# Optimization experiments

Hardware: AMD Instinct MI355X
Metric: run time of the kernel (lower is better)

The kernel has to match this reference:

```python
import jax, jax.numpy as jnp
import numpy as np

N, FIN, C1, C2 = 4096, 6, 1000, 1000
K1, K2, KR = 3, 6, 3
NR, S, NCLS = 20, 205, 40


def pairwise_adj(x):
    # exp(-squared_euclidean_distance), RGCNN pairwise_distance
    inner = -2.0 * jnp.einsum('bnf,bmf->bnm', x, x)
    sq = jnp.sum(x * x, axis=-1, keepdims=True)
    return jnp.exp(-(sq + inner + jnp.swapaxes(sq, 1, 2)))


def knn_sparsify(adj, k):
    # keep top-k similarities per row, zero the rest (get_one_matrix_knn)
    vals, idx = jax.lax.top_k(adj, k)
    B, n, _ = adj.shape
    b = jnp.arange(B)[:, None, None]
    r = jnp.arange(n)[None, :, None]
    return jnp.zeros_like(adj).at[b, r, idx].set(vals)


def get_laplacian(W):
    # normalized Laplacian L = I - D^-1/2 W D^-1/2
    dinv = 1.0 / jnp.sqrt(jnp.sum(W, axis=-1))
    Lnorm = W * dinv[:, :, None] * dinv[:, None, :]
    return jnp.eye(W.shape[-1], dtype=W.dtype)[None] - Lnorm


def cheb_conv(x, L, W, b, K):
    # Chebyshev recursion: Tx0=x, Tx1=Lx, Txk=2L Tx_{k-1} - Tx_{k-2}
    Tx = [x]
    if K > 1:
        Tx.append(jnp.einsum('bnm,bmf->bnf', L, x))
    for _ in range(2, K):
        Tx.append(2.0 * jnp.einsum('bnm,bmf->bnf', L, Tx[-1]) - Tx[-2])
    xhat = jnp.concatenate(Tx, axis=-1)  # [B, N, K*Fin]
    return jnp.einsum('bnf,fo->bno', xhat, W) + b


def setup_inputs() -> dict:
    key = jax.random.key(0)
    ks = jax.random.split(key, 16)
    sc = 0.02
    return {
        'x': jax.random.normal(ks[0], (1, N, FIN), jnp.float32),
        'k': 40,
        'batch_size': 1,
        'num_points': N,
        'vertices_Reeb': jax.random.normal(ks[1], (NR, 3), jnp.float32),
        'laplacian_Reeb': jax.random.normal(ks[2], (NR, NR), jnp.float32),
        'sccs': jax.random.randint(ks[3], (NR, S), 0, N),
        'W1': jax.random.normal(ks[4], (K1 * FIN, C1), jnp.float32) * sc,
        'b1': jnp.zeros((C1,), jnp.float32),
        'W2': jax.random.normal(ks[5], (K2 * C1, C2), jnp.float32) * sc,
        'b2': jnp.zeros((C2,), jnp.float32),
        'Wr': jax.random.normal(ks[6], (KR * C1, C2), jnp.float32) * sc,
        'br': jnp.zeros((C2,), jnp.float32),
        'fc1_w': jax.random.normal(ks[7], (2 * C2, 512), jnp.float32) * sc,
        'fc1_b': jnp.zeros((512,), jnp.float32),
        'fc2_w': jax.random.normal(ks[8], (512, 128), jnp.float32) * sc,
        'fc2_b': jnp.zeros((128,), jnp.float32),
        'fc3_w': jax.random.normal(ks[9], (128, NCLS), jnp.float32) * sc,
        'fc3_b': jnp.zeros((NCLS,), jnp.float32),
    }


def reference(x, k, batch_size, num_points, vertices_Reeb, laplacian_Reeb, sccs,
              W1, b1, W2, b2, Wr, br, fc1_w, fc1_b, fc2_w, fc2_b, fc3_w, fc3_b):
    fro = lambda a: jnp.linalg.norm(a.reshape(-1))
    regs = []
    # dynamic KNN graph + Laplacian (no_grad in original -> stop_gradient)
    L = jax.lax.stop_gradient(get_laplacian(knn_sparsify(pairwise_adj(x), k)))
    out = jax.nn.relu(cheb_conv(x, L, W1, b1, K1))  # [1, N, 1000]
    regs.append(fro(jnp.einsum('bnc,bnm,bmf->bcf', out, L, x)))
    # Reeb pooling: max over each scc's node features (sample 0)
    vfr = jnp.max(out[0][sccs], axis=1)[None]  # [1, 20, 1000]
    L_reeb = laplacian_Reeb[None]
    # second dynamic graph on features
    L2 = jax.lax.stop_gradient(get_laplacian(knn_sparsify(pairwise_adj(out), k)))
    out2 = jax.nn.relu(cheb_conv(out, L2, W2, b2, K2))
    regs.append(fro(jnp.einsum('bnc,bnm,bmf->bcf', out2, L2, x)))
    out_reeb = jax.nn.relu(cheb_conv(vfr, L_reeb, Wr, br, KR))
    out_m = jnp.max(out2, axis=1)       # [1, 1000]
    reeb_m = jnp.max(out_reeb, axis=1)  # [1, 1000]
    of = jnp.concatenate([reeb_m, out_m], axis=1)  # [1, 2000]
    of = jax.nn.relu(of @ fc1_w + fc1_b)
    regs += [jnp.linalg.norm(fc1_w.T[0]) ** 2, fc1_b[0] ** 2]
    of = jax.nn.relu(of @ fc2_w + fc2_b)
    regs += [jnp.linalg.norm(fc2_w.T[0]) ** 2, fc2_b[0] ** 2]
    of = of @ fc3_w + fc3_b  # [1, 40]
    regs += [jnp.linalg.norm(fc3_w.T[0]) ** 2, fc3_b[0] ** 2]
    return of, jnp.stack(regs)
```

## Files before the change

### kernel.cpp

```cpp
#include <hip/hip_runtime.h>
#include <math.h>

#define N4    4096
#define FDIM  6
#define CC    1000
#define KP    1024
#define KP6   (6 * KP)
#define KNN   40
#define NRB   20
#define SSC   205

typedef __attribute__((ext_vector_type(8))) short bf16x8;
typedef __attribute__((ext_vector_type(4))) float f32x4;

__device__ __forceinline__ unsigned short f2bf(float f) {
    unsigned u = __float_as_uint(f);
    u = (u + 0x7fffu + ((u >> 16) & 1u)) >> 16;
    return (unsigned short)u;
}
__device__ __forceinline__ float bf2f(short s) {
    return __uint_as_float(((unsigned)(unsigned short)s) << 16);
}

__device__ __forceinline__ unsigned d2key(float d) {
    unsigned u = __float_as_uint(d);
    return ((int)u < 0) ? u : (~u) ^ 0x80000000u;
}
__device__ __forceinline__ float key2d(unsigned k) {
    unsigned u = (k >> 31) ? k : (~k) ^ 0x80000000u;
    return __uint_as_float(u);
}

__device__ __forceinline__ void gload16(const unsigned short* g, short* l) {
    __builtin_amdgcn_global_load_lds(
        (const __attribute__((address_space(1))) unsigned int*)g,
        (__attribute__((address_space(3))) unsigned int*)l, 16, 0, 0);
}


__global__ __launch_bounds__(256) void sqx_kernel(const float* __restrict__ x,
                                                  float* __restrict__ sq1,
                                                  float* __restrict__ xhat) {
    int n = blockIdx.x * blockDim.x + threadIdx.x;
    if (n >= N4) return;
    float s = 0.f;
#pragma unroll
    for (int f = 0; f < FDIM; ++f) {
        float v = x[n * FDIM + f];
        s += v * v;
        xhat[n * 18 + f] = v;
    }
    sq1[n] = s;
}


#define NHC 8
#define HSTRIDE 257

struct TopkSh {
    unsigned sv[N4];
    int hist[NHC * HSTRIDE];
    int sc[256];
    float red[8];
    unsigned short cidx[N4];
    unsigned s_pfx;
    int s_need, s_cnt, s_m;
};

__device__ __forceinline__ void topk_prep(TopkSh& sh, int t) {
    if (t == 0) { sh.s_pfx = 0u; sh.s_need = KNN; sh.s_cnt = 0; sh.s_m = 0; }
    for (int q = t; q < NHC * HSTRIDE; q += 512) sh.hist[q] = 0;
}

__device__ __forceinline__ void hist_pick(TopkSh& sh, int level, int t, int lane, int w, int nc) {
    if (t < 256) {
        int cnt = 0;
        for (int c = 0; c < nc; ++c) cnt += sh.hist[c * HSTRIDE + t];
        sh.sc[t] = cnt;
    }
    __syncthreads();
    if (w == 0) {
        int need = sh.s_need;
        unsigned pfx = sh.s_pfx;
        int c0 = sh.sc[4 * lane + 0], c1 = sh.sc[4 * lane + 1];
        int c2 = sh.sc[4 * lane + 2], c3 = sh.sc[4 * lane + 3];
        int s = c0 + c1 + c2 + c3;
        int suf = s;
#pragma unroll
        for (int off = 1; off < 64; off <<= 1) {
            int ov = __shfl_down(suf, off, 64);
            if (lane + off < 64) suf += ov;
        }
        int above = suf - s;
        int i3 = above + c3, i2 = i3 + c2, i1 = i2 + c1, i0 = i1 + c0;
        if (i3 >= need && i3 - c3 < need) { sh.s_need = need - (i3 - c3); sh.s_pfx = pfx | ((unsigned)(4 * lane + 3) << level); }
        if (i2 >= need && i2 - c2 < need) { sh.s_need = need - (i2 - c2); sh.s_pfx = pfx | ((unsigned)(4 * lane + 2) << level); }
        if (i1 >= need && i1 - c1 < need) { sh.s_need = need - (i1 - c1); sh.s_pfx = pfx | ((unsigned)(4 * lane + 1) << level); }
        if (i0 >= need && i0 - c0 < need) { sh.s_need = need - (i0 - c0); sh.s_pfx = pfx | ((unsigned)(4 * lane + 0) << level); }
    }
    __syncthreads();
}

template<int LASTLEVEL>
__device__ void topk_core(TopkSh& sh, int n, int* __restrict__ idx,
                          float* __restrict__ val, float* __restrict__ rowsum) {
    int t = threadIdx.x, lane = t & 63, w = t >> 6;
    __syncthreads();
    hist_pick(sh, 24, t, lane, w, NHC);
    unsigned b1 = sh.s_pfx >> 24;

    for (int i = t; i < N4; i += 512) {
        unsigned u = sh.sv[i];
        bool isc = ((u >> 24) >= b1);
        unsigned long long mm = __ballot(isc);
        int cw = __popcll(mm);
        int base = 0;
        if (lane == 0 && cw) base = atomicAdd(&sh.s_m, cw);
        base = __shfl(base, 0);
        if (isc) sh.cidx[base + __popcll(mm & ((1ull << lane) - 1ull))] = (unsigned short)i;
    }
    __syncthreads();
    int mcnt = sh.s_m;

    for (int level = 16; level >= LASTLEVEL; level -= 8) {
        for (int q = t; q < HSTRIDE; q += 512) sh.hist[q] = 0;
        __syncthreads();
        unsigned pfx = sh.s_pfx;
        for (int j = t; j < mcnt; j += 512) {
            unsigned u = sh.sv[sh.cidx[j]];
            if ((u >> (level + 8)) == (pfx >> (level + 8)))
                atomicAdd(&sh.hist[(u >> level) & 255], 1);
        }
        __syncthreads();
        hist_pick(sh, level, t, lane, w, 1);
    }
    unsigned Tbits = sh.s_pfx;
    if (LASTLEVEL == 16) Tbits |= (Tbits & 0x80000000u) ? 0u : 0xFFFFu;
    float Tf = __expf(-key2d(Tbits));
    int needEq = sh.s_need;

    float psum = 0.f;
    for (int j = t; j < mcnt; j += 512) {
        unsigned u = sh.sv[sh.cidx[j]];
        if (u > Tbits) {
            int p = atomicAdd(&sh.s_cnt, 1);
            float v = __expf(-key2d(u));
            idx[(size_t)n * KNN + p] = (int)sh.cidx[j];
            val[(size_t)n * KNN + p] = v;
            psum += v;
        }
    }
#pragma unroll
    for (int o = 32; o; o >>= 1) psum += __shfl_down(psum, o);
    if (lane == 0) sh.red[w] = psum;
    __syncthreads();
    if (t == 0) {
        float s = 0.f;
#pragma unroll
        for (int q = 0; q < 8; ++q) s += sh.red[q];
        rowsum[n] = s + (float)needEq * Tf;
    }

    if (t < 64) {
        int filled = KNN - needEq;
        for (int ib = 0; ib < N4 && filled < KNN; ib += 64) {
            bool eq = (sh.sv[ib + t] == Tbits);
            unsigned long long m = __ballot(eq);
            int pre = __popcll(m & ((1ull << t) - 1ull));
            if (eq && (filled + pre) < KNN) {
                idx[(size_t)n * KNN + filled + pre] = ib + t;
                val[(size_t)n * KNN + filled + pre] = Tf;
            }
            filled += __popcll(m);
        }
    }
}

__global__ __launch_bounds__(512) void topk_fused1(const float* __restrict__ x,
                                                   const float* __restrict__ sq1,
                                                   int* __restrict__ idx, float* __restrict__ val,
                                                   float* __restrict__ rowsum) {
    __shared__ TopkSh sh;
    __shared__ float xn[FDIM];
    __shared__ float sns;
    int n = blockIdx.x;
    int t = threadIdx.x;
    if (t < FDIM) xn[t] = x[n * FDIM + t];
    if (t == FDIM) sns = sq1[n];
    topk_prep(sh, t);
    __syncthreads();
    float x0 = xn[0], x1 = xn[1], x2 = xn[2], x3 = xn[3], x4 = xn[4], x5 = xn[5];
    float sn = sns;
    int* hw = &sh.hist[(t & 7) * HSTRIDE];
    for (int i = t; i < N4; i += 512) {
        const float2* xi = (const float2*)(x + i * FDIM);
        float2 p0 = xi[0], p1 = xi[1], p2 = xi[2];
        float d = x0 * p0.x + x1 * p0.y + x2 * p1.x + x3 * p1.y + x4 * p2.x + x5 * p2.y;
        float e = sn + sq1[i] - 2.f * d;
        unsigned k = d2key(e);
        sh.sv[i] = k;
        atomicAdd(&hw[k >> 24], 1);
    }
    topk_core<0>(sh, n, idx, val, rowsum);
}

__global__ __launch_bounds__(512) void topk_radix(const unsigned short* __restrict__ S,
                                                  int* __restrict__ idx, float* __restrict__ val,
                                                  float* __restrict__ rowsum) {
    __shared__ TopkSh sh;
    int n = blockIdx.x;
    int t = threadIdx.x;
    topk_prep(sh, t);
    const unsigned short* row = S + (size_t)n * N4;
    bf16x8 a = *(const bf16x8*)(row + 8 * t);
    __syncthreads();
    int* hw = &sh.hist[(t & 7) * HSTRIDE];
#pragma unroll
    for (int q = 0; q < 8; ++q) {
        unsigned k = d2key(bf2f(a[q]));
        sh.sv[8 * t + q] = k;
        atomicAdd(&hw[k >> 24], 1);
    }
    topk_core<16>(sh, n, idx, val, rowsum);
}

__global__ __launch_bounds__(256) void wnorm_kernel(float* __restrict__ wv,
                                                    const int* __restrict__ idx,
                                                    const float* __restrict__ rs) {
    int i = blockIdx.x * 256 + threadIdx.x;
    if (i >= N4 * KNN) return;
    int n = i / KNN;
    wv[i] = wv[i] * rsqrtf(rs[n]) * rsqrtf(rs[idx[i]]);
}

__global__ __launch_bounds__(64) void spmv_cheb(const float* __restrict__ Tc,
                                                const float* __restrict__ Tp,
                                                float* __restrict__ Tn,
                                                const int* __restrict__ idx,
                                                const float* __restrict__ wv,
                                                int F, int sC, int sP, int sN,
                                                float a, float b) {
    __shared__ int   si[KNN];
    __shared__ float sw[KNN];
    int n = blockIdx.x;
    if (threadIdx.x < KNN) {
        si[threadIdx.x] = idx[(size_t)n * KNN + threadIdx.x];
        sw[threadIdx.x] = wv[(size_t)n * KNN + threadIdx.x];
    }
    __syncthreads();
    for (int c = threadIdx.x; c < F; c += blockDim.x) {
        float s = 0.f;
#pragma unroll 8
        for (int j = 0; j < KNN; ++j) s += sw[j] * Tc[(size_t)si[j] * sC + c];
        float v = a * (Tc[(size_t)n * sC + c] - s);
        if (b != 0.f) v -= b * Tp[(size_t)n * sP + c];
        Tn[(size_t)n * sN + c] = v;
    }
}

__global__ __launch_bounds__(256) void spmv_cheb_bf(const unsigned short* __restrict__ Tcbf,
                                                    const unsigned short* __restrict__ Tpbf,
                                                    unsigned short* __restrict__ Tnbf,
                                                    const int* __restrict__ idx,
                                                    const float* __restrict__ wv,
                                                    float a, float b) {
    __shared__ int   si[KNN];
    __shared__ float sw[KNN];
    __shared__ float part[3][64][9];
    int n = blockIdx.x;
    int t = threadIdx.x;
    int tt = t & 63, g = t >> 6;
    if (t < KNN) {
        si[t] = idx[(size_t)n * KNN + t];
        sw[t] = wv[(size_t)n * KNN + t];
    }
    __syncthreads();
    int c = blockIdx.y * 512 + tt * 8;
    float acc0 = 0, acc1 = 0, acc2 = 0, acc3 = 0, acc4 = 0, acc5 = 0, acc6 = 0, acc7 = 0;
    int j0 = g * 10;
#pragma unroll
    for (int j = j0; j < j0 + 10; ++j) {
        bf16x8 v = *(const bf16x8*)(Tcbf + (size_t)si[j] * KP6 + c);
        float wj = sw[j];
        acc0 += wj * bf2f(v[0]); acc1 += wj * bf2f(v[1]);
        acc2 += wj * bf2f(v[2]); acc3 += wj * bf2f(v[3]);
        acc4 += wj * bf2f(v[4]); acc5 += wj * bf2f(v[5]);
        acc6 += wj * bf2f(v[6]); acc7 += wj * bf2f(v[7]);
    }
    if (g) {
        float* p = part[g - 1][tt];
        p[0] = acc0; p[1] = acc1; p[2] = acc2; p[3] = acc3;
        p[4] = acc4; p[5] = acc5; p[6] = acc6; p[7] = acc7;
    }
    __syncthreads();
    if (g == 0) {
#pragma unroll
        for (int pg = 0; pg < 3; ++pg) {
            const float* p = part[pg][tt];
            acc0 += p[0]; acc1 += p[1]; acc2 += p[2]; acc3 += p[3];
            acc4 += p[4]; acc5 += p[5]; acc6 += p[6]; acc7 += p[7];
        }
        bf16x8 tc = *(const bf16x8*)(Tcbf + (size_t)n * KP6 + c);
        float o0 = a * (bf2f(tc[0]) - acc0), o1 = a * (bf2f(tc[1]) - acc1);
        float o2 = a * (bf2f(tc[2]) - acc2), o3 = a * (bf2f(tc[3]) - acc3);
        float o4 = a * (bf2f(tc[4]) - acc4), o5 = a * (bf2f(tc[5]) - acc5);
        float o6 = a * (bf2f(tc[6]) - acc6), o7 = a * (bf2f(tc[7]) - acc7);
        if (b != 0.f) {
            bf16x8 tp = *(const bf16x8*)(Tpbf + (size_t)n * KP6 + c);
            o0 -= b * bf2f(tp[0]); o1 -= b * bf2f(tp[1]);
            o2 -= b * bf2f(tp[2]); o3 -= b * bf2f(tp[3]);
            o4 -= b * bf2f(tp[4]); o5 -= b * bf2f(tp[5]);
            o6 -= b * bf2f(tp[6]); o7 -= b * bf2f(tp[7]);
        }
        bf16x8 ob;
        ob[0] = (short)f2bf(o0); ob[1] = (short)f2bf(o1);
        ob[2] = (short)f2bf(o2); ob[3] = (short)f2bf(o3);
        ob[4] = (short)f2bf(o4); ob[5] = (short)f2bf(o5);
        ob[6] = (short)f2bf(o6); ob[7] = (short)f2bf(o7);
        *(bf16x8*)(Tnbf + (size_t)n * KP6 + c) = ob;
    }
}


__global__ __launch_bounds__(256) void cvt_bf16_kernel(const float* __restrict__ in,
                                                       unsigned short* __restrict__ out) {
    int i = blockIdx.x * 256 + threadIdx.x;
    int r = i >> 7, g = i & 127;
    bf16x8 v;
    if (g < 125) {
        float4 a = *(const float4*)(in + (size_t)r * CC + g * 8);
        float4 b = *(const float4*)(in + (size_t)r * CC + g * 8 + 4);
        v[0] = (short)f2bf(a.x); v[1] = (short)f2bf(a.y);
        v[2] = (short)f2bf(a.z); v[3] = (short)f2bf(a.w);
        v[4] = (short)f2bf(b.x); v[5] = (short)f2bf(b.y);
        v[6] = (short)f2bf(b.z); v[7] = (short)f2bf(b.w);
    } else {
#pragma unroll
        for (int q = 0; q < 8; ++q) v[q] = 0;
    }
    *(bf16x8*)(out + (size_t)r * KP6 + g * 8) = v;
}

__global__ __launch_bounds__(256) void w2t_kernel(const float* __restrict__ W2,
                                                  unsigned short* __restrict__ out) {
    __shared__ unsigned short tile[64][65];
    int t = threadIdx.x;
    int k0 = blockIdx.x * 64, n0 = blockIdx.y * 64, s = blockIdx.z;
#pragma unroll
    for (int p = 0; p < 16; ++p) {
        int i = p * 256 + t;
        int kk = i >> 6, nn = i & 63;
        int k = k0 + kk, n = n0 + nn;
        float v = (k < CC && n < CC) ? W2[((size_t)s * CC + k) * CC + n] : 0.f;
        tile[kk][nn] = f2bf(v);
    }
    __syncthreads();
#pragma unroll
    for (int p = 0; p < 16; ++p) {
        int i = p * 256 + t;
        int nn = i >> 6, kk = i & 63;
        out[(size_t)(n0 + nn) * KP6 + (size_t)s * KP + k0 + kk] = tile[kk][nn];
    }
}


#define LDT 32
#define SP2 136
#define SP 264
#define ABUF (128 * LDT)
#define BBUF (256 * LDT)

template<int STR>
__device__ __forceinline__ void gemm_core128_bk64(const unsigned short* __restrict__ Ag,
                                                  const unsigned short* __restrict__ Bg,
                                                  short* sm, int t,
                                                  int kbeg, int kend,
                                                  f32x4 (&acc)[4][4]) {
    int l = t & 63, w = t >> 6;
    int wm = (w >> 1) * 64, wn = (w & 1) * 64;
    int lr = l & 15, lq8 = (l >> 4) * 8;
    short* A0 = sm;
    short* A1 = sm + ABUF;
    short* B0 = sm + 2 * ABUF;
    short* B1 = sm + 3 * ABUF;
    size_t ga0 = (size_t)(32 * w + (l >> 2)) * STR + (l & 3) * 8;
    size_t ga1 = ga0 + (size_t)16 * STR;
    int lo = (32 * w) * LDT;
    for (int k0 = kbeg; k0 < kend; k0 += 64) {
        gload16(Ag + ga0 + k0,      A0 + lo);
        gload16(Ag + ga1 + k0,      A0 + lo + 16 * LDT);
        gload16(Ag + ga0 + k0 + 32, A1 + lo);
        gload16(Ag + ga1 + k0 + 32, A1 + lo + 16 * LDT);
        gload16(Bg + ga0 + k0,      B0 + lo);
        gload16(Bg + ga1 + k0,      B0 + lo + 16 * LDT);
        gload16(Bg + ga0 + k0 + 32, B1 + lo);
        gload16(Bg + ga1 + k0 + 32, B1 + lo + 16 * LDT);
        __syncthreads();
        bf16x8 af[4], bfr[4];
#pragma unroll
        for (int mi = 0; mi < 4; ++mi)
            af[mi] = *(const bf16x8*)&A0[(wm + mi * 16 + lr) * LDT + lq8];
#pragma unroll
        for (int ni = 0; ni < 4; ++ni)
            bfr[ni] = *(const bf16x8*)&B0[(wn + ni * 16 + lr) * LDT + lq8];
#pragma unroll
        for (int mi = 0; mi < 4; ++mi)
#pragma unroll
            for (int ni = 0; ni < 4; ++ni)
                acc[mi][ni] = __builtin_amdgcn_mfma_f32_16x16x32_bf16(af[mi], bfr[ni], acc[mi][ni], 0, 0, 0);
#pragma unroll
        for (int mi = 0; mi < 4; ++mi)
            af[mi] = *(const bf16x8*)&A1[(wm + mi * 16 + lr) * LDT + lq8];
#pragma unroll
        for (int ni = 0; ni < 4; ++ni)
            bfr[ni] = *(const bf16x8*)&B1[(wn + ni * 16 + lr) * LDT + lq8];
#pragma unroll
        for (int mi = 0; mi < 4; ++mi)
#pragma unroll
            for (int ni = 0; ni < 4; ++ni)
                acc[mi][ni] = __builtin_amdgcn_mfma_f32_16x16x32_bf16(af[mi], bfr[ni], acc[mi][ni], 0, 0, 0);
        __syncthreads();
    }
}

template<int STR>
__device__ __forceinline__ void gemm_core256(const unsigned short* __restrict__ Ag,
                                             const unsigned short* __restrict__ Bg,
                                             short* As, short* Bs, int t,
                                             int kbeg, int kend,
                                             f32x4 (&acc)[4][8]) {
    int l = t & 63, w = t >> 6;
    int wm = (w >> 1) * 64, wn = (w & 1) * 128;
    int lr = l & 15, lq8 = (l >> 4) * 8;
    size_t soff = (size_t)(16 * w + (l >> 2)) * STR + (l & 3) * 8;
    const unsigned short* gA = Ag + soff;
    const unsigned short* gB = Bg + soff;
    int wb = w * 512;
    gload16(gA + kbeg, As + wb);
    gload16(gA + kbeg + (size_t)64 * STR, As + wb + 64 * LDT);
    gload16(gB + kbeg, Bs + wb);
    gload16(gB + kbeg + (size_t)64 * STR, Bs + wb + 64 * LDT);
    gload16(gB + kbeg + (size_t)128 * STR, Bs + wb + 128 * LDT);
    gload16(gB + kbeg + (size_t)192 * STR, Bs + wb + 192 * LDT);
    __syncthreads();
    int cur = 0;
    for (int k0 = kbeg; k0 < kend; k0 += 32) {
        int nxt = cur ^ 1;
        if (k0 + 32 < kend) {
            short* nA = As + nxt * ABUF + wb;
            short* nB = Bs + nxt * BBUF + wb;
            gload16(gA + k0 + 32, nA);
            gload16(gA + k0 + 32 + (size_t)64 * STR, nA + 64 * LDT);
            gload16(gB + k0 + 32, nB);
            gload16(gB + k0 + 32 + (size_t)64 * STR, nB + 64 * LDT);
            gload16(gB + k0 + 32 + (size_t)128 * STR, nB + 128 * LDT);
            gload16(gB + k0 + 32 + (size_t)192 * STR, nB + 192 * LDT);
        }
        const short* cA = As + cur * ABUF;
        const short* cB = Bs + cur * BBUF;
        bf16x8 af[4], bfr[8];
#pragma unroll
        for (int mi = 0; mi < 4; ++mi)
            af[mi] = *(const bf16x8*)&cA[(wm + mi * 16 + lr) * LDT + lq8];
#pragma unroll
        for (int ni = 0; ni < 8; ++ni)
            bfr[ni] = *(const bf16x8*)&cB[(wn + ni * 16 + lr) * LDT + lq8];
#pragma unroll
        for (int mi = 0; mi < 4; ++mi)
#pragma unroll
            for (int ni = 0; ni < 8; ++ni)
                acc[mi][ni] = __builtin_amdgcn_mfma_f32_16x16x32_bf16(af[mi], bfr[ni], acc[mi][ni], 0, 0, 0);
        __syncthreads();
        cur = nxt;
    }
}

__global__ __launch_bounds__(256) void gemm_mfma_big(const unsigned short* __restrict__ A,
                                                     const unsigned short* __restrict__ B,
                                                     unsigned short* __restrict__ Cp) {
    __shared__ short smem[4 * ABUF];
    int t = threadIdx.x;
    int m0 = blockIdx.x * 128, n0 = blockIdx.y * 128;
    int kz = blockIdx.z;
    unsigned short* C = Cp + (size_t)kz * N4 * CC;
    f32x4 acc[4][4] = {};
    gemm_core128_bk64<KP6>(A + (size_t)m0 * KP6, B + (size_t)n0 * KP6, smem, t,
                           kz * 2 * KP, kz * 2 * KP + 2 * KP, acc);
    int l = t & 63, w = t >> 6;
    int wn = (w & 1) * 64;
    int lr = l & 15, lq4 = (l >> 4) * 4;
    int lrow = (w >> 1) * 16 + lq4;
#pragma unroll
    for (int mi = 0; mi < 4; ++mi) {
        __syncthreads();
#pragma unroll
        for (int ni = 0; ni < 4; ++ni) {
            int col = wn + ni * 16 + lr;
            f32x4 v = acc[mi][ni];
#pragma unroll
            for (int r = 0; r < 4; ++r) smem[(lrow + r) * SP2 + col] = (short)f2bf(v[r]);
        }
        __syncthreads();
#pragma unroll
        for (int q = 0; q < 2; ++q) {
            int row = q * 16 + (t >> 4);
            int col = (t & 15) * 8;
            int gm = m0 + (row >> 4) * 64 + mi * 16 + (row & 15);
            int gn = n0 + col;
            if (gn < CC) {
                bf16x8 vv = *(bf16x8*)&smem[row * SP2 + col];
                *(bf16x8*)(C + (size_t)gm * CC + gn) = vv;
            }
        }
    }
}

__global__ __launch_bounds__(256) void bias_relu_merge(const unsigned short* __restrict__ Cp,
                                                       const float* __restrict__ b2,
                                                       float* __restrict__ out2) {
    size_t i8 = (size_t)blockIdx.x * 256 + threadIdx.x;
    if (i8 >= (size_t)N4 * CC / 8) return;
    size_t i = i8 * 8;
    int c = (int)(i % CC);
    const size_t S = (size_t)N4 * CC;
    float s[8] = {};
#pragma unroll
    for (int z = 0; z < 3; ++z) {
        bf16x8 v = *(const bf16x8*)(Cp + z * S + i);
#pragma unroll
        for (int q = 0; q < 8; ++q) s[q] += bf2f(v[q]);
    }
    float4 o0, o1;
    o0.x = fmaxf(s[0] + b2[c + 0], 0.f); o0.y = fmaxf(s[1] + b2[c + 1], 0.f);
    o0.z = fmaxf(s[2] + b2[c + 2], 0.f); o0.w = fmaxf(s[3] + b2[c + 3], 0.f);
    o1.x = fmaxf(s[4] + b2[c + 4], 0.f); o1.y = fmaxf(s[5] + b2[c + 5], 0.f);
    o1.z = fmaxf(s[6] + b2[c + 6], 0.f); o1.w = fmaxf(s[7] + b2[c + 7], 0.f);
    *(float4*)(out2 + i) = o0;
    *(float4*)(out2 + i + 4) = o1;
}

__global__ __launch_bounds__(256, 2) void gram2_mfma(const unsigned short* __restrict__ Tall,
                                                     const float* __restrict__ sq2,
                                                     unsigned short* __restrict__ S) {
    __shared__ short smem[2 * ABUF + 2 * BBUF];
    short* As = smem;
    short* Bs = smem + 2 * ABUF;
    int t = threadIdx.x;
    int m0 = blockIdx.x * 128, n0 = blockIdx.y * 256;
    f32x4 acc[4][8] = {};
    gemm_core256<KP6>(Tall + (size_t)m0 * KP6, Tall + (size_t)n0 * KP6, As, Bs, t, 0, KP, acc);
    int l = t & 63, w = t >> 6;
    int wn = (w & 1) * 128;
    int lr = l & 15, lq4 = (l >> 4) * 4;
    int lrow = (w >> 1) * 16 + lq4;
#pragma unroll
    for (int mi = 0; mi < 4; ++mi) {
        __syncthreads();
        int mbase = m0 + (w >> 1) * 64 + mi * 16 + lq4;
#pragma unroll
        for (int ni = 0; ni < 8; ++ni) {
            int col = wn + ni * 16 + lr;
            float sn = sq2[n0 + col];
            f32x4 v = acc[mi][ni];
#pragma unroll
            for (int r = 0; r < 4; ++r)
                smem[(lrow + r) * SP + col] = (short)f2bf(sq2[mbase + r] + sn - 2.f * v[r]);
        }
        __syncthreads();
#pragma unroll
        for (int q = 0; q < 4; ++q) {
            int row = q * 8 + (t >> 5);
            int col = (t & 31) * 8;
            int gm = m0 + (row >> 4) * 64 + mi * 16 + (row & 15);
            int gn = n0 + col;
            bf16x8 vv = *(bf16x8*)&smem[row * SP + col];
            *(bf16x8*)(S + (size_t)gm * N4 + gn) = vv;
        }
    }
}


__global__ __launch_bounds__(256) void cheb1_out_kernel(const float* __restrict__ xhat,
                                                        const float* __restrict__ W1,
                                                        const float* __restrict__ b1,
                                                        float* __restrict__ outF) {
    __shared__ float xh[16][18];
    int n0 = blockIdx.x * 16;
    int tid = threadIdx.x;
    for (int i = tid; i < 16 * 18; i += 256) xh[i / 18][i % 18] = xhat[(size_t)n0 * 18 + i];
    __syncthreads();
    for (int c0 = 0; c0 < CC; c0 += 256) {
        int c = c0 + tid;
        if (c < CC) {
            float acc[16];
#pragma unroll
            for (int r = 0; r < 16; ++r) acc[r] = 0.f;
            for (int f = 0; f < 18; ++f) {
                float wv = W1[(size_t)f * CC + c];
#pragma unroll
                for (int r = 0; r < 16; ++r) acc[r] += xh[r][f] * wv;
            }
            float bb = b1[c];
#pragma unroll
            for (int r = 0; r < 16; ++r)
                outF[(size_t)(n0 + r) * CC + c] = fmaxf(acc[r] + bb, 0.f);
        }
    }
}


__global__ __launch_bounds__(256) void matT6_partial(const float* __restrict__ O,
                                                     const float* __restrict__ T, int ts,
                                                     float* __restrict__ M) {
    __shared__ float sT[128][6];
    int t = threadIdx.x;
    int c = blockIdx.x * 256 + t;
    int n0 = blockIdx.y * 128;
    for (int i = t; i < 128 * 6; i += 256) {
        int nn = i / 6, f = i % 6;
        sT[nn][f] = T[(size_t)(n0 + nn) * ts + f];
    }
    __syncthreads();
    if (c >= CC) return;
    float a0 = 0, a1 = 0, a2 = 0, a3 = 0, a4 = 0, a5 = 0;
    for (int nn = 0; nn < 128; ++nn) {
        float o = O[(size_t)(n0 + nn) * CC + c];
        a0 += o * sT[nn][0]; a1 += o * sT[nn][1]; a2 += o * sT[nn][2];
        a3 += o * sT[nn][3]; a4 += o * sT[nn][4]; a5 += o * sT[nn][5];
    }
    atomicAdd(&M[0 * CC + c], a0);
    atomicAdd(&M[1 * CC + c], a1);
    atomicAdd(&M[2 * CC + c], a2);
    atomicAdd(&M[3 * CC + c], a3);
    atomicAdd(&M[4 * CC + c], a4);
    atomicAdd(&M[5 * CC + c], a5);
}

__global__ __launch_bounds__(256) void fro_kernel(const float* __restrict__ M, float* __restrict__ dst) {
    __shared__ float red[256];
    int t = threadIdx.x;
    int i = blockIdx.x * 256 + t;
    float v = (i < 6 * CC) ? M[i] : 0.f;
    red[t] = v * v;
    __syncthreads();
    for (int o = 128; o; o >>= 1) { if (t < o) red[t] += red[t + o]; __syncthreads(); }
    if (t == 0) atomicAdd(dst, red[0]);
}


__global__ __launch_bounds__(256) void vfr_kernel(const float* __restrict__ outF,
                                                  const int* __restrict__ sccs,
                                                  float* __restrict__ vfr) {
    int r = blockIdx.y;
    int c = blockIdx.x * 256 + threadIdx.x;
    if (c >= CC) return;
    int s0 = blockIdx.z * 41;
    float m = 0.f;
    for (int s = s0; s < s0 + 41; ++s) {
        int n = sccs[r * SSC + s];
        m = fmaxf(m, outF[(size_t)n * CC + c]);
    }
    atomicMax((int*)&vfr[(size_t)r * CC + c], __float_as_int(m));
}

__global__ __launch_bounds__(256) void sq2_kernel(const float* __restrict__ outF,
                                                  float* __restrict__ sq2) {
    int lane = threadIdx.x & 63, w = threadIdx.x >> 6;
    int n = blockIdx.x * 4 + w;
    const float* row = outF + (size_t)n * CC;
    float s = 0.f;
    for (int i = lane; i < CC; i += 64) { float v = row[i]; s += v * v; }
#pragma unroll
    for (int o = 32; o; o >>= 1) s += __shfl_down(s, o);
    if (lane == 0) sq2[n] = s;
}

__global__ __launch_bounds__(256) void colmax_kernel(const float* __restrict__ O,
                                                     float* __restrict__ dst) {
    int c = blockIdx.x * 256 + threadIdx.x;
    if (c >= CC) return;
    int n0 = blockIdx.y * 64;
    float m = 0.f;
    for (int n = n0; n < n0 + 64; ++n) m = fmaxf(m, O[(size_t)n * CC + c]);
    atomicMax((int*)&dst[c], __float_as_int(m));
}


__global__ __launch_bounds__(256) void reeb_mm_kernel(const float* __restrict__ Lr,
                                                      const float* __restrict__ Vin,
                                                      const float* __restrict__ Vsub,
                                                      float* __restrict__ Vout, float a2) {
    int c = blockIdx.x * 256 + threadIdx.x;
    if (c >= CC) return;
    int r = blockIdx.y;
    float s = 0.f;
#pragma unroll
    for (int j = 0; j < NRB; ++j) s += Lr[r * NRB + j] * Vin[(size_t)j * CC + c];
    float v = a2 * s;
    if (Vsub) v -= Vsub[(size_t)r * CC + c];
    Vout[(size_t)r * CC + c] = v;
}

#define RKC 25
__global__ __launch_bounds__(256) void reeb_conv_splitk(const float* __restrict__ vfr,
                                                        const float* __restrict__ tr1,
                                                        const float* __restrict__ tr2,
                                                        const float* __restrict__ Wr,
                                                        float* __restrict__ rpre) {
    __shared__ float sA[NRB][RKC];
    int t = threadIdx.x;
    int kbase = blockIdx.y * RKC;
    for (int i = t; i < NRB * RKC; i += 256) {
        int r = i / RKC, kk = i % RKC;
        int kg = kbase + kk;
        float v;
        if (kg < CC)           v = vfr[(size_t)r * CC + kg];
        else if (kg < 2 * CC)  v = tr1[(size_t)r * CC + kg - CC];
        else                   v = tr2[(size_t)r * CC + kg - 2 * CC];
        sA[r][kk] = v;
    }
    __syncthreads();
    int c = blockIdx.x * 256 + t;
    if (c >= CC) return;
    float acc[NRB];
#pragma unroll
    for (int r = 0; r < NRB; ++r) acc[r] = 0.f;
    for (int kk = 0; kk < RKC; ++kk) {
        float wv = Wr[(size_t)(kbase + kk) * CC + c];
#pragma unroll
        for (int r = 0; r < NRB; ++r) acc[r] += sA[r][kk] * wv;
    }
#pragma unroll
    for (int r = 0; r < NRB; ++r) atomicAdd(&rpre[(size_t)r * CC + c], acc[r]);
}

__global__ __launch_bounds__(256) void reeb_max_kernel(const float* __restrict__ pre,
                                                       const float* __restrict__ br,
                                                       float* __restrict__ rbm) {
    int c = blockIdx.x * 256 + threadIdx.x;
    if (c >= CC) return;
    float bb = br[c];
    float m = 0.f;
    for (int r = 0; r < NRB; ++r) m = fmaxf(m, fmaxf(pre[(size_t)r * CC + c] + bb, 0.f));
    rbm[c] = m;
}


__global__ __launch_bounds__(256) void fc1_kernel(const float* __restrict__ rbm,
                                                  const float* __restrict__ otm,
                                                  const float* __restrict__ w,
                                                  float* __restrict__ h1pre) {
    int j = blockIdx.x * 256 + threadIdx.x;
    if (j >= 512) return;
    int i0 = blockIdx.y * 250;
    float s = 0.f;
    for (int i = i0; i < i0 + 250; ++i) {
        float v = (i < CC) ? rbm[i] : otm[i - CC];
        s += v * w[(size_t)i * 512 + j];
    }
    atomicAdd(&h1pre[j], s);
}

__global__ __launch_bounds__(512) void fc23_kernel(const float* __restrict__ h1pre,
                                                   const float* __restrict__ b1f,
                                                   const float* __restrict__ w2,
                                                   const float* __restrict__ b2f,
                                                   const float* __restrict__ w3,
                                                   const float* __restrict__ b3f,
                                                   float* __restrict__ dout) {
    __shared__ float h1[512];
    __shared__ float h2[128];
    int t = threadIdx.x;
    h1[t] = fmaxf(h1pre[t] + b1f[t], 0.f);
    __syncthreads();
    if (t < 128) {
        float s = b2f[t];
        for (int i = 0; i < 512; ++i) s += h1[i] * w2[(size_t)i * 128 + t];
        h2[t] = fmaxf(s, 0.f);
    }
    __syncthreads();
    if (t < 40) {
        float s = b3f[t];
        for (int i = 0; i < 128; ++i) s += h2[i] * w3[(size_t)i * 40 + t];
        dout[t] = s;
    }
}

__global__ __launch_bounds__(256) void finalize_kernel(const float* __restrict__ racc,
                                                       const float* __restrict__ f1w,
                                                       const float* __restrict__ f1b,
                                                       const float* __restrict__ f2w,
                                                       const float* __restrict__ f2b,
                                                       const float* __restrict__ f3w,
                                                       const float* __restrict__ f3b,
                                                       float* __restrict__ dout) {
    __shared__ float red[256];
    __shared__ float res[3];
    int t = threadIdx.x;
    float s1 = 0.f, s2 = 0.f, s3 = 0.f;
    for (int i = t; i < 2000; i += 256) { float v = f1w[(size_t)i * 512]; s1 += v * v; }
    for (int i = t; i < 512; i += 256) { float v = f2w[(size_t)i * 128]; s2 += v * v; }
    if (t < 128) { float v = f3w[(size_t)t * 40]; s3 = v * v; }

    red[t] = s1; __syncthreads();
    for (int o = 128; o; o >>= 1) { if (t < o) red[t] += red[t + o]; __syncthreads(); }
    if (t == 0) res[0] = red[0];
    __syncthreads();
    red[t] = s2; __syncthreads();
    for (int o = 128; o; o >>= 1) { if (t < o) red[t] += red[t + o]; __syncthreads(); }
    if (t == 0) res[1] = red[0];
    __syncthreads();
    red[t] = s3; __syncthreads();
    for (int o = 128; o; o >>= 1) { if (t < o) red[t] += red[t + o]; __syncthreads(); }
    if (t == 0) res[2] = red[0];
    __syncthreads();

    if (t == 0) {
        dout[40] = sqrtf(racc[0]);
        dout[41] = sqrtf(racc[1]);
        dout[42] = res[0];
        dout[43] = f1b[0] * f1b[0];
        dout[44] = res[1];
        dout[45] = f2b[0] * f2b[0];
        dout[46] = res[2];
        dout[47] = f3b[0] * f3b[0];
    }
}


extern "C" void kernel_launch(void* const* d_in, const int* in_sizes, int n_in,
                              void* d_out, int out_size, void* d_ws, size_t ws_size,
                              hipStream_t stream) {
    const float* x    = (const float*)d_in[0];
    const float* Lr   = (const float*)d_in[5];
    const int*   sccs = (const int*)d_in[6];
    const float* W1   = (const float*)d_in[7];
    const float* b1   = (const float*)d_in[8];
    const float* W2   = (const float*)d_in[9];
    const float* b2   = (const float*)d_in[10];
    const float* Wr   = (const float*)d_in[11];
    const float* br   = (const float*)d_in[12];
    const float* f1w  = (const float*)d_in[13];
    const float* f1b  = (const float*)d_in[14];
    const float* f2w  = (const float*)d_in[15];
    const float* f2b  = (const float*)d_in[16];
    const float* f3w  = (const float*)d_in[17];
    const float* f3b  = (const float*)d_in[18];
    float* dout = (float*)d_out;

    char* ws = (char*)d_ws;
    size_t off = 0;
    auto alloc = [&](size_t bytes) -> char* {
        char* p = ws + off;
        off = (off + bytes + 255) & ~(size_t)255;
        return p;
    };
    float* outF = (float*)alloc((size_t)N4 * CC * 4);
    unsigned short* Cpb = (unsigned short*)alloc((size_t)6 * N4 * CC * 2);
    unsigned short* Sb  = (unsigned short*)alloc((size_t)N4 * N4 * 2);
    unsigned short* Tall = (unsigned short*)alloc((size_t)N4 * KP6 * 2);
    unsigned short* W2T6 = Sb;
    float* xhat = (float*)alloc((size_t)N4 * 18 * 4);
    float* sq1  = (float*)alloc(N4 * 4);
    float* sq2  = (float*)alloc(N4 * 4);
    float* rs1  = (float*)alloc(N4 * 4);
    float* rs2  = (float*)alloc(N4 * 4);
    float* wv1  = (float*)alloc((size_t)N4 * KNN * 4);
    float* wv2  = (float*)alloc((size_t)N4 * KNN * 4);
    int*   ix1  = (int*)alloc((size_t)N4 * KNN * 4);
    int*   ix2  = (int*)alloc((size_t)N4 * KNN * 4);
    float* t2x  = (float*)alloc((size_t)N4 * FDIM * 4);
    float* tr1  = (float*)alloc((size_t)NRB * CC * 4);
    float* tr2  = (float*)alloc((size_t)NRB * CC * 4);
    char*  zbase = ws + off;
    float* Mb   = (float*)alloc(6 * CC * 4);
    float* Mb2  = (float*)alloc(6 * CC * 4);
    float* rbm  = (float*)alloc(CC * 4);
    float* otm  = (float*)alloc(CC * 4);
    float* h1p  = (float*)alloc(512 * 4);
    float* racc = (float*)alloc(64 * 4);
    float* rpre = (float*)alloc((size_t)NRB * CC * 4);
    float* vfr  = (float*)alloc((size_t)NRB * CC * 4);
    size_t zlen = (size_t)((ws + off) - zbase);
    if (off > ws_size) return;

    hipMemsetAsync(zbase, 0, zlen, stream);

    sqx_kernel<<<(N4 + 255) / 256, 256, 0, stream>>>(x, sq1, xhat);
    topk_fused1<<<N4, 512, 0, stream>>>(x, sq1, ix1, wv1, rs1);
    wnorm_kernel<<<(N4 * KNN + 255) / 256, 256, 0, stream>>>(wv1, ix1, rs1);

    spmv_cheb<<<N4, 64, 0, stream>>>(xhat, xhat, xhat + 6, ix1, wv1, FDIM, 18, 18, 18, 1.f, 0.f);
    spmv_cheb<<<N4, 64, 0, stream>>>(xhat + 6, xhat, xhat + 12, ix1, wv1, FDIM, 18, 18, 18, 2.f, 1.f);
    cheb1_out_kernel<<<N4 / 16, 256, 0, stream>>>(xhat, W1, b1, outF);

    matT6_partial<<<dim3(4, 32), 256, 0, stream>>>(outF, xhat + 6, 18, Mb);
    fro_kernel<<<24, 256, 0, stream>>>(Mb, racc + 0);

    vfr_kernel<<<dim3(4, NRB, 5), 256, 0, stream>>>(outF, sccs, vfr);

    sq2_kernel<<<N4 / 4, 256, 0, stream>>>(outF, sq2);
    cvt_bf16_kernel<<<N4 * 128 / 256, 256, 0, stream>>>(outF, Tall);
    gram2_mfma<<<dim3(N4 / 128, N4 / 256), 256, 0, stream>>>(Tall, sq2, Sb);
    topk_radix<<<N4, 512, 0, stream>>>(Sb, ix2, wv2, rs2);
    wnorm_kernel<<<(N4 * KNN + 255) / 256, 256, 0, stream>>>(wv2, ix2, rs2);

    w2t_kernel<<<dim3(16, 16, 6), 256, 0, stream>>>(W2, W2T6);

    spmv_cheb<<<N4, 64, 0, stream>>>(x, x, t2x, ix2, wv2, FDIM, FDIM, FDIM, FDIM, 1.f, 0.f);

    spmv_cheb_bf<<<dim3(N4, 2), 256, 0, stream>>>(Tall + 0 * KP, Tall + 0 * KP, Tall + 1 * KP, ix2, wv2, 1.f, 0.f);
    spmv_cheb_bf<<<dim3(N4, 2), 256, 0, stream>>>(Tall + 1 * KP, Tall + 0 * KP, Tall + 2 * KP, ix2, wv2, 2.f, 1.f);
    spmv_cheb_bf<<<dim3(N4, 2), 256, 0, stream>>>(Tall + 2 * KP, Tall + 1 * KP, Tall + 3 * KP, ix2, wv2, 2.f, 1.f);
    spmv_cheb_bf<<<dim3(N4, 2), 256, 0, stream>>>(Tall + 3 * KP, Tall + 2 * KP, Tall + 4 * KP, ix2, wv2, 2.f, 1.f);
    spmv_cheb_bf<<<dim3(N4, 2), 256, 0, stream>>>(Tall + 4 * KP, Tall + 3 * KP, Tall + 5 * KP, ix2, wv2, 2.f, 1.f);

    gemm_mfma_big<<<dim3(N4 / 128, 8, 3), 256, 0, stream>>>(Tall, W2T6, Cpb);
    bias_relu_merge<<<(int)(((size_t)N4 * CC / 8 + 255) / 256), 256, 0, stream>>>(Cpb, b2, outF);

    matT6_partial<<<dim3(4, 32), 256, 0, stream>>>(outF, t2x, FDIM, Mb2);
    fro_kernel<<<24, 256, 0, stream>>>(Mb2, racc + 1);

    colmax_kernel<<<dim3(4, 64), 256, 0, stream>>>(outF, otm);

    reeb_mm_kernel<<<dim3(4, NRB), 256, 0, stream>>>(Lr, vfr, nullptr, tr1, 1.f);
    reeb_mm_kernel<<<dim3(4, NRB), 256, 0, stream>>>(Lr, tr1, vfr, tr2, 2.f);
    reeb_conv_splitk<<<dim3(4, 120), 256, 0, stream>>>(vfr, tr1, tr2, Wr, rpre);
    reeb_max_kernel<<<4, 256, 0, stream>>>(rpre, br, rbm);

    fc1_kernel<<<dim3(2, 8), 256, 0, stream>>>(rbm, otm, f1w, h1p);
    fc23_kernel<<<1, 512, 0, stream>>>(h1p, f1b, f2w, f2b, f3w, f3b, dout);
    finalize_kernel<<<1, 256, 0, stream>>>(racc, f1w, f1b, f2w, f2b, f3w, f3b, dout);
}
```

Baseline: 627.7 us.

## Cache high key bits for radix top-k candidates and parallelize tie fill

The radix top-k now stores the upper 16 key bits of each candidate in a compact shared array. Later histogram passes and the final selection read that array instead of doing an indirect gather into the full key array, and the 16-bit level is unrolled explicitly. The first-level histogram uses run-length-merged atomics with fewer per-thread histogram copies, and the tie-fill scan is spread over all waves with a prefix count instead of one wave scanning serially. This adds shared memory and a barrier, and halving the histogram copies may increase atomic contention.

```diff
diff --git a/kernel.cpp b/kernel.cpp
--- a/kernel.cpp
+++ b/kernel.cpp
@@ -54,7 +54,7 @@
 }
 
 
-#define NHC 8
+#define NHC 4
 #define HSTRIDE 257
 
 struct TopkSh {
@@ -63,6 +63,7 @@
     int sc[256];
     float red[8];
     unsigned short cidx[N4];
+    unsigned short cv16[N4];
     unsigned s_pfx;
     int s_need, s_cnt, s_m;
 };
@@ -117,37 +118,80 @@
         int base = 0;
         if (lane == 0 && cw) base = atomicAdd(&sh.s_m, cw);
         base = __shfl(base, 0);
-        if (isc) sh.cidx[base + __popcll(mm & ((1ull << lane) - 1ull))] = (unsigned short)i;
+        if (isc) {
+            int p = base + __popcll(mm & ((1ull << lane) - 1ull));
+            sh.cidx[p] = (unsigned short)i;
+            sh.cv16[p] = (unsigned short)(u >> 16);
+        }
     }
     __syncthreads();
     int mcnt = sh.s_m;
 
-    for (int level = 16; level >= LASTLEVEL; level -= 8) {
+    for (int q = t; q < HSTRIDE; q += 512) sh.hist[q] = 0;
+    __syncthreads();
+    {
+        unsigned pb = sh.s_pfx >> 24;
+        for (int j = t; j < mcnt; j += 512) {
+            unsigned v = sh.cv16[j];
+            if ((v >> 8) == pb) atomicAdd(&sh.hist[v & 255], 1);
+        }
+    }
+    __syncthreads();
+    hist_pick(sh, 16, t, lane, w, 1);
+
+    if (LASTLEVEL == 0) {
         for (int q = t; q < HSTRIDE; q += 512) sh.hist[q] = 0;
         __syncthreads();
-        unsigned pfx = sh.s_pfx;
-        for (int j = t; j < mcnt; j += 512) {
-            unsigned u = sh.sv[sh.cidx[j]];
-            if ((u >> (level + 8)) == (pfx >> (level + 8)))
-                atomicAdd(&sh.hist[(u >> level) & 255], 1);
-        }
-        __syncthreads();
-        hist_pick(sh, level, t, lane, w, 1);
-    }
+        {
+            unsigned short p16 = (unsigned short)(sh.s_pfx >> 16);
+            for (int j = t; j < mcnt; j += 512) {
+                if (sh.cv16[j] == p16) {
+                    unsigned u = sh.sv[sh.cidx[j]];
+                    atomicAdd(&sh.hist[(u >> 8) & 255], 1);
+                }
+            }
+        }
+        __syncthreads();
+        hist_pick(sh, 8, t, lane, w, 1);
+
+        for (int q = t; q < HSTRIDE; q += 512) sh.hist[q] = 0;
+        __syncthreads();
+        {
+            unsigned pfx = sh.s_pfx;
+            unsigned short p16 = (unsigned short)(pfx >> 16);
+            for (int j = t; j < mcnt; j += 512) {
+                if (sh.cv16[j] == p16) {
+                    unsigned u = sh.sv[sh.cidx[j]];
+                    if ((u >> 8) == (pfx >> 8)) atomicAdd(&sh.hist[u & 255], 1);
+                }
+            }
+        }
+        __syncthreads();
+        hist_pick(sh, 0, t, lane, w, 1);
+    }
+
     unsigned Tbits = sh.s_pfx;
     if (LASTLEVEL == 16) Tbits |= (Tbits & 0x80000000u) ? 0u : 0xFFFFu;
     float Tf = __expf(-key2d(Tbits));
     int needEq = sh.s_need;
 
     float psum = 0.f;
+    unsigned short T16 = (unsigned short)(Tbits >> 16);
     for (int j = t; j < mcnt; j += 512) {
-        unsigned u = sh.sv[sh.cidx[j]];
-        if (u > Tbits) {
-            int p = atomicAdd(&sh.s_cnt, 1);
-            float v = __expf(-key2d(u));
-            idx[(size_t)n * KNN + p] = (int)sh.cidx[j];
-            val[(size_t)n * KNN + p] = v;
-            psum += v;
+        unsigned short v = sh.cv16[j];
+        if (v >= T16) {
+            unsigned u;
+            if (LASTLEVEL == 16)
+                u = ((unsigned)v << 16) | ((v & 0x8000u) ? 0u : 0xFFFFu);
+            else
+                u = sh.sv[sh.cidx[j]];
+            if (u > Tbits) {
+                int p = atomicAdd(&sh.s_cnt, 1);
+                float fv = __expf(-key2d(u));
+                idx[(size_t)n * KNN + p] = (int)sh.cidx[j];
+                val[(size_t)n * KNN + p] = fv;
+                psum += fv;
+            }
         }
     }
 #pragma unroll
@@ -161,17 +205,31 @@
         rowsum[n] = s + (float)needEq * Tf;
     }
 
-    if (t < 64) {
-        int filled = KNN - needEq;
-        for (int ib = 0; ib < N4 && filled < KNN; ib += 64) {
-            bool eq = (sh.sv[ib + t] == Tbits);
-            unsigned long long m = __ballot(eq);
-            int pre = __popcll(m & ((1ull << t) - 1ull));
-            if (eq && (filled + pre) < KNN) {
-                idx[(size_t)n * KNN + filled + pre] = ib + t;
-                val[(size_t)n * KNN + filled + pre] = Tf;
+    {
+        int filled0 = KNN - needEq;
+        int base_i = w * 512;
+        int cnt = 0;
+#pragma unroll
+        for (int q = 0; q < 8; ++q) {
+            bool eq = (sh.sv[base_i + q * 64 + lane] == Tbits);
+            cnt += __popcll(__ballot(eq));
+        }
+        if (lane == 0) sh.sc[w] = cnt;
+        __syncthreads();
+        int pre = 0;
+        for (int q = 0; q < w; ++q) pre += sh.sc[q];
+        if (pre < needEq) {
+            int run = pre;
+            for (int q = 0; q < 8 && run < needEq; ++q) {
+                bool eq = (sh.sv[base_i + q * 64 + lane] == Tbits);
+                unsigned long long m = __ballot(eq);
+                int lpre = __popcll(m & ((1ull << lane) - 1ull));
+                if (eq && run + lpre < needEq) {
+                    idx[(size_t)n * KNN + filled0 + run + lpre] = base_i + q * 64 + lane;
+                    val[(size_t)n * KNN + filled0 + run + lpre] = Tf;
+                }
+                run += __popcll(m);
             }
-            filled += __popcll(m);
         }
     }
 }
@@ -191,7 +249,8 @@
     __syncthreads();
     float x0 = xn[0], x1 = xn[1], x2 = xn[2], x3 = xn[3], x4 = xn[4], x5 = xn[5];
     float sn = sns;
-    int* hw = &sh.hist[(t & 7) * HSTRIDE];
+    int* hw = &sh.hist[(t & 3) * HSTRIDE];
+    unsigned prevb = 0xFFFFFFFFu; int rl = 0;
     for (int i = t; i < N4; i += 512) {
         const float2* xi = (const float2*)(x + i * FDIM);
         float2 p0 = xi[0], p1 = xi[1], p2 = xi[2];
@@ -199,8 +258,11 @@
         float e = sn + sq1[i] - 2.f * d;
         unsigned k = d2key(e);
         sh.sv[i] = k;
-        atomicAdd(&hw[k >> 24], 1);
-    }
+        unsigned b = k >> 24;
+        if (b == prevb) ++rl;
+        else { if (rl) atomicAdd(&hw[prevb], rl); prevb = b; rl = 1; }
+    }
+    if (rl) atomicAdd(&hw[prevb], rl);
     topk_core<0>(sh, n, idx, val, rowsum);
 }
 
@@ -214,13 +276,17 @@
     const unsigned short* row = S + (size_t)n * N4;
     bf16x8 a = *(const bf16x8*)(row + 8 * t);
     __syncthreads();
-    int* hw = &sh.hist[(t & 7) * HSTRIDE];
+    int* hw = &sh.hist[(t & 3) * HSTRIDE];
+    unsigned prevb = 0xFFFFFFFFu; int rl = 0;
 #pragma unroll
     for (int q = 0; q < 8; ++q) {
         unsigned k = d2key(bf2f(a[q]));
         sh.sv[8 * t + q] = k;
-        atomicAdd(&hw[k >> 24], 1);
-    }
+        unsigned b = k >> 24;
+        if (b == prevb) ++rl;
+        else { if (rl) atomicAdd(&hw[prevb], rl); prevb = b; rl = 1; }
+    }
+    if (rl) atomicAdd(&hw[prevb], rl);
     topk_core<16>(sh, n, idx, val, rowsum);
 }
 
```

Result: faster. 604.6 us (-3.7%).
